# Kernel optimization log

Hardware: AMD Instinct MI355X
Metric: run time of the kernel (lower is better)

## Reference

```python
import jax, jax.numpy as jnp
import numpy as np

B, N, C_IN, C_OUT, R_IN, R_OUT, NUM_PSI, E = 4, 1024, 128, 256, 32, 32, 2, 65536


def psi(x, src, dst, W, b):
    # GIN-style GNN layer: aggregate neighbors via scatter-add, then linear+relu
    agg = jax.ops.segment_sum(x[src], dst, num_segments=x.shape[0])
    return jax.nn.relu((x + agg) @ W + b)


def setup_inputs() -> dict:
    key = jax.random.key(0)
    ks = jax.random.split(key, 12)
    inp = {
        'x_s': jax.random.normal(ks[0], (B * N, C_IN), jnp.float32),
        'edge_index_s': jax.random.randint(ks[1], (2, E), 0, B * N, jnp.int32),
        'x_t': jax.random.normal(ks[2], (B * N, C_IN), jnp.float32),
        'edge_index_t': jax.random.randint(ks[3], (2, E), 0, B * N, jnp.int32),
        'r': jax.random.normal(ks[4], (NUM_PSI, B, N, R_IN), jnp.float32),
        'W1': jax.random.normal(ks[5], (C_IN, C_OUT), jnp.float32) * (0.2 / np.sqrt(C_IN)),
        'b1': jnp.zeros((C_OUT,), jnp.float32),
        'Wp': jax.random.normal(ks[6], (NUM_PSI, R_IN, R_OUT), jnp.float32) * (1.0 / np.sqrt(R_IN)),
        'bp': jnp.zeros((NUM_PSI, R_OUT), jnp.float32),
        'Wm1': jax.random.normal(ks[7], (R_OUT, R_OUT), jnp.float32) * (1.0 / np.sqrt(R_OUT)),
        'bm1': jnp.zeros((R_OUT,), jnp.float32),
        'Wm2': jax.random.normal(ks[8], (R_OUT, 1), jnp.float32) * (1.0 / np.sqrt(R_OUT)),
        'bm2': jnp.zeros((1,), jnp.float32),
        'sum_weights': jnp.ones((NUM_PSI + 1,), jnp.float32),
    }
    return inp


def reference(x_s, edge_index_s, x_t, edge_index_t, r, W1, b1, Wp, bp, Wm1, bm1, Wm2, bm2, sum_weights):
    src_s, dst_s = edge_index_s[0], edge_index_s[1]
    src_t, dst_t = edge_index_t[0], edge_index_t[1]
    # psi_1 node embeddings, then dense-batch (equal-size graphs -> masks all true)
    h_s = psi(x_s, src_s, dst_s, W1, b1).reshape(B, N, C_OUT)
    h_t = psi(x_t, src_t, dst_t, W1, b1).reshape(B, N, C_OUT)
    S_hat = jnp.einsum('bsc,btc->bst', h_s, h_t)  # [B, N_s, N_t]
    S_0 = jax.nn.softmax(S_hat, axis=-1)
    S_stack = []
    for i in range(NUM_PSI):  # structurally distinct psi modules
        S = jax.nn.softmax(S_hat, axis=-1)
        r_s = r[i]  # [B, N, R_IN] random node indicators
        r_t = jnp.einsum('bst,bsr->btr', S, r_s)
        o_s = psi(r_s.reshape(B * N, R_IN), src_s, dst_s, Wp[i], bp[i]).reshape(B, N, R_OUT)
        o_t = psi(r_t.reshape(B * N, R_IN), src_t, dst_t, Wp[i], bp[i]).reshape(B, N, R_OUT)
        D = o_s[:, :, None, :] - o_t[:, None, :, :]  # [B, N_s, N_t, R_OUT]
        upd = (jax.nn.relu(D @ Wm1 + bm1) @ Wm2 + bm2)[..., 0]
        S_hat = S_hat + upd
        S_stack.append(jax.nn.softmax(S_hat, axis=-1))
    S_final = sum_weights[0] * S_0
    for i in range(NUM_PSI):
        S_final = S_final + sum_weights[i + 1] * S_stack[i]
    return jax.nn.softmax(S_final.reshape(B * N, N), axis=-1)
```

## Files before the change

kernel.cpp:

```cpp
#include <hip/hip_runtime.h>
#include <hip/hip_bf16.h>

#define NBATCH 4
#define NSEQ   1024
#define BNN    4096
#define CIN    128
#define COUT   256
#define RDIM   32
#define NEDGE  65536

__global__ void edge_hist(const int* __restrict__ ei_s, const int* __restrict__ ei_t,
                          int* __restrict__ cnt) {
    int gid = blockIdx.x * blockDim.x + threadIdx.x;
    int list = gid >> 16;
    int e = gid & (NEDGE - 1);
    const int* ei = list ? ei_t : ei_s;
    atomicAdd(&cnt[list * BNN + ei[NEDGE + e]], 1);
}

__global__ void edge_scan(const int* __restrict__ cnt, int* __restrict__ offs,
                          int* __restrict__ cursor) {
    __shared__ int sums[256];
    int list = blockIdx.x;
    int tid = threadIdx.x;
    int local[16];
    int s = 0;
#pragma unroll
    for (int k = 0; k < 16; k++) { local[k] = cnt[list * BNN + tid * 16 + k]; s += local[k]; }
    sums[tid] = s;
    __syncthreads();
    for (int off = 1; off < 256; off <<= 1) {
        int v = 0;
        if (tid >= off) v = sums[tid - off];
        __syncthreads();
        if (tid >= off) sums[tid] += v;
        __syncthreads();
    }
    int run = tid ? sums[tid - 1] : 0;
#pragma unroll
    for (int k = 0; k < 16; k++) {
        offs[list * (BNN + 1) + tid * 16 + k] = run;
        cursor[list * BNN + tid * 16 + k] = run;
        run += local[k];
    }
    if (tid == 255) offs[list * (BNN + 1) + BNN] = run;
}

__global__ void edge_place(const int* __restrict__ ei_s, const int* __restrict__ ei_t,
                           int* __restrict__ cursor, int* __restrict__ ssrc) {
    int gid = blockIdx.x * blockDim.x + threadIdx.x;
    int list = gid >> 16;
    int e = gid & (NEDGE - 1);
    const int* ei = list ? ei_t : ei_s;
    int dst = ei[NEDGE + e], src = ei[e];
    int p = atomicAdd(&cursor[list * BNN + dst], 1);
    ssrc[list * NEDGE + p] = src;
}

__global__ void gather_agg128(const float* __restrict__ x_s, const float* __restrict__ x_t,
                              const int* __restrict__ offs, const int* __restrict__ ssrc,
                              float* __restrict__ t_s, float* __restrict__ t_t) {
    __shared__ int sl[128];
    int node = blockIdx.x & (BNN - 1);
    int list = blockIdx.x >> 12;
    const float* x = list ? x_t : x_s;
    float* t = list ? t_t : t_s;
    int c = threadIdx.x;
    int beg = offs[list * (BNN + 1) + node], end = offs[list * (BNN + 1) + node + 1];
    float acc = x[(size_t)node * CIN + c];
    for (int base = beg; base < end; base += 128) {
        int cnt = min(128, end - base);
        __syncthreads();
        if (c < cnt) sl[c] = ssrc[list * NEDGE + base + c];
        __syncthreads();
        int e = 0;
        for (; e + 4 <= cnt; e += 4) {
            int n0 = sl[e], n1 = sl[e + 1], n2 = sl[e + 2], n3 = sl[e + 3];
            acc += x[(size_t)n0 * CIN + c] + x[(size_t)n1 * CIN + c]
                 + x[(size_t)n2 * CIN + c] + x[(size_t)n3 * CIN + c];
        }
        for (; e < cnt; e++) acc += x[(size_t)sl[e] * CIN + c];
    }
    t[(size_t)node * CIN + c] = acc;
}

__global__ void gather_agg32(const float* __restrict__ rs, const float* __restrict__ rtin,
                             const int* __restrict__ offs, const int* __restrict__ ssrc,
                             float* __restrict__ trs, float* __restrict__ trt) {
    int list = blockIdx.y;
    int node = blockIdx.x * 8 + (threadIdx.x >> 5);
    int c = threadIdx.x & 31;
    const float* in = list ? rtin : rs;
    float* outp = list ? trt : trs;
    int beg = offs[list * (BNN + 1) + node], end = offs[list * (BNN + 1) + node + 1];
    float acc = in[(size_t)node * RDIM + c];
    for (int e = beg; e < end; e++)
        acc += in[(size_t)ssrc[list * NEDGE + e] * RDIM + c];
    outp[(size_t)node * RDIM + c] = acc;
}

__global__ void psi1_gemm(const float* __restrict__ t_s, const float* __restrict__ t_t,
                          const float* __restrict__ W1, const float* __restrict__ b1,
                          float* __restrict__ h_s, float* __restrict__ h_t) {
    __shared__ float rows[8][CIN];
    int half = blockIdx.x >> 9;
    const float* t = half ? t_t : t_s;
    float* h = half ? h_t : h_s;
    int r0 = (blockIdx.x & 511) * 8;
    int tid = threadIdx.x;
    {
        int rr = tid >> 5, c4 = (tid & 31) << 2;
        *(float4*)&rows[rr][c4] = *(const float4*)(t + (size_t)(r0 + rr) * CIN + c4);
    }
    __syncthreads();
    float acc[8];
    float bias = b1[tid];
#pragma unroll
    for (int r = 0; r < 8; r++) acc[r] = bias;
    for (int k = 0; k < CIN; k++) {
        float w = W1[k * COUT + tid];
#pragma unroll
        for (int r = 0; r < 8; r++) acc[r] = fmaf(rows[r][k], w, acc[r]);
    }
#pragma unroll
    for (int r = 0; r < 8; r++)
        h[(size_t)(r0 + r) * COUT + tid] = fmaxf(acc[r], 0.f);
}

__global__ __launch_bounds__(256) void shat_gemm(const float* __restrict__ hs,
                                                 const float* __restrict__ ht,
                                                 float* __restrict__ Sh) {
    __shared__ float As[16][68];
    __shared__ float Bs[16][68];
    int flat = blockIdx.x;
    int swz = (flat & 7) * 128 + (flat >> 3);
    int bx = swz & 15, by = (swz >> 4) & 15, bz = swz >> 8;
    int b  = bz;
    int s0 = by * 64, t0 = bx * 64;
    const float* A  = hs + (size_t)b * NSEQ * COUT;
    const float* Bm = ht + (size_t)b * NSEQ * COUT;
    int tid = threadIdx.x;
    int tx = tid & 15, ty = tid >> 4;
    int lr = tid >> 2, lk = (tid & 3) << 2;
    const float* Ap = A  + (size_t)(s0 + lr) * COUT + lk;
    const float* Bp = Bm + (size_t)(t0 + lr) * COUT + lk;
    float4 a0 = *(const float4*)(Ap);
    float4 b0 = *(const float4*)(Bp);
    float acc[4][4] = {};
    for (int kp = 0; kp < 16; kp++) {
        __syncthreads();
        As[lk + 0][lr] = a0.x; As[lk + 1][lr] = a0.y;
        As[lk + 2][lr] = a0.z; As[lk + 3][lr] = a0.w;
        Bs[lk + 0][lr] = b0.x; Bs[lk + 1][lr] = b0.y;
        Bs[lk + 2][lr] = b0.z; Bs[lk + 3][lr] = b0.w;
        __syncthreads();
        if (kp < 15) {
            a0 = *(const float4*)(Ap + (kp + 1) * 16);
            b0 = *(const float4*)(Bp + (kp + 1) * 16);
        }
#pragma unroll
        for (int k = 0; k < 16; k++) {
            float av[4], bv[4];
            *(float4*)&av[0] = *(const float4*)&As[k][ty * 4];
            *(float4*)&bv[0] = *(const float4*)&Bs[k][tx * 4];
#pragma unroll
            for (int i = 0; i < 4; i++)
#pragma unroll
                for (int j = 0; j < 4; j++)
                    acc[i][j] = fmaf(av[i], bv[j], acc[i][j]);
        }
    }
#pragma unroll
    for (int i = 0; i < 4; i++) {
        float4 v = make_float4(acc[i][0], acc[i][1], acc[i][2], acc[i][3]);
        *(float4*)(Sh + ((size_t)b * NSEQ + s0 + ty * 4 + i) * NSEQ + t0 + tx * 4) = v;
    }
}

__global__ void softmax_stats(const float* __restrict__ Sh, float* __restrict__ mstat,
                              float* __restrict__ istat) {
    int row = blockIdx.x, tid = threadIdx.x;
    float4 v = *(const float4*)(Sh + (size_t)row * NSEQ + tid * 4);
    float m = fmaxf(fmaxf(v.x, v.y), fmaxf(v.z, v.w));
#pragma unroll
    for (int o = 32; o; o >>= 1) m = fmaxf(m, __shfl_xor(m, o));
    __shared__ float redm[4], reds[4];
    int wid = tid >> 6, lane = tid & 63;
    if (lane == 0) redm[wid] = m;
    __syncthreads();
    m = fmaxf(fmaxf(redm[0], redm[1]), fmaxf(redm[2], redm[3]));
    float s = __expf(v.x - m) + __expf(v.y - m) + __expf(v.z - m) + __expf(v.w - m);
#pragma unroll
    for (int o = 32; o; o >>= 1) s += __shfl_xor(s, o);
    if (lane == 0) reds[wid] = s;
    __syncthreads();
    if (tid == 0) {
        float tot = reds[0] + reds[1] + reds[2] + reds[3];
        mstat[row] = m;
        istat[row] = 1.0f / tot;
    }
}

__global__ void softmax_final3(const float* __restrict__ Sh0, const float* __restrict__ Sh1,
                               const float* __restrict__ Sh2, const float* __restrict__ m0a,
                               const float* __restrict__ i0a, const float* __restrict__ m1a,
                               const float* __restrict__ i1a, const float* __restrict__ sw,
                               float* __restrict__ out) {
    int row = blockIdx.x, tid = threadIdx.x;
    __shared__ float red[4];
    int wid = tid >> 6, lane = tid & 63;
    float4 v0 = *(const float4*)(Sh0 + (size_t)row * NSEQ + tid * 4);
    float4 v1 = *(const float4*)(Sh1 + (size_t)row * NSEQ + tid * 4);
    float4 v2 = *(const float4*)(Sh2 + (size_t)row * NSEQ + tid * 4);
    float m2 = fmaxf(fmaxf(v2.x, v2.y), fmaxf(v2.z, v2.w));
#pragma unroll
    for (int o = 32; o; o >>= 1) m2 = fmaxf(m2, __shfl_xor(m2, o));
    if (lane == 0) red[wid] = m2;
    __syncthreads();
    m2 = fmaxf(fmaxf(red[0], red[1]), fmaxf(red[2], red[3]));
    __syncthreads();
    float4 e2;
    e2.x = __expf(v2.x - m2); e2.y = __expf(v2.y - m2);
    e2.z = __expf(v2.z - m2); e2.w = __expf(v2.w - m2);
    float s2 = e2.x + e2.y + e2.z + e2.w;
#pragma unroll
    for (int o = 32; o; o >>= 1) s2 += __shfl_xor(s2, o);
    if (lane == 0) red[wid] = s2;
    __syncthreads();
    s2 = red[0] + red[1] + red[2] + red[3];
    __syncthreads();
    float w0 = sw[0] * i0a[row], w1 = sw[1] * i1a[row], w2 = sw[2] / s2;
    float m0 = m0a[row], m1 = m1a[row];
    float4 f;
    f.x = fmaf(w0, __expf(v0.x - m0), fmaf(w1, __expf(v1.x - m1), w2 * e2.x));
    f.y = fmaf(w0, __expf(v0.y - m0), fmaf(w1, __expf(v1.y - m1), w2 * e2.y));
    f.z = fmaf(w0, __expf(v0.z - m0), fmaf(w1, __expf(v1.z - m1), w2 * e2.z));
    f.w = fmaf(w0, __expf(v0.w - m0), fmaf(w1, __expf(v1.w - m1), w2 * e2.w));
    float mf = fmaxf(fmaxf(f.x, f.y), fmaxf(f.z, f.w));
#pragma unroll
    for (int o = 32; o; o >>= 1) mf = fmaxf(mf, __shfl_xor(mf, o));
    if (lane == 0) red[wid] = mf;
    __syncthreads();
    mf = fmaxf(fmaxf(red[0], red[1]), fmaxf(red[2], red[3]));
    __syncthreads();
    float4 ef;
    ef.x = __expf(f.x - mf); ef.y = __expf(f.y - mf);
    ef.z = __expf(f.z - mf); ef.w = __expf(f.w - mf);
    float sf = ef.x + ef.y + ef.z + ef.w;
#pragma unroll
    for (int o = 32; o; o >>= 1) sf += __shfl_xor(sf, o);
    if (lane == 0) red[wid] = sf;
    __syncthreads();
    sf = red[0] + red[1] + red[2] + red[3];
    float inv = 1.0f / sf;
    float4 sv = make_float4(ef.x * inv, ef.y * inv, ef.z * inv, ef.w * inv);
    *(float4*)(out + (size_t)row * NSEQ + tid * 4) = sv;
}

__global__ void rt_part(const float* __restrict__ Sh, const float* __restrict__ mstat,
                        const float* __restrict__ istat, const float* __restrict__ rs,
                        float* __restrict__ part) {
    __shared__ float rsld[64][33];
    __shared__ float ml[64], il[64];
    int b = blockIdx.z, t0 = blockIdx.y * 128, s0 = blockIdx.x * 64;
    int tid = threadIdx.x;
    if (tid < 64) ml[tid] = mstat[b * NSEQ + s0 + tid];
    else if (tid < 128) il[tid - 64] = istat[b * NSEQ + s0 + tid - 64];
#pragma unroll
    for (int q = 0; q < 2; q++) {
        int lid = (tid << 1) + q;
        int srow = lid >> 3, c4 = (lid & 7) << 2;
        float4 v = *(const float4*)(rs + ((size_t)b * NSEQ + s0 + srow) * RDIM + c4);
        rsld[srow][c4] = v.x; rsld[srow][c4 + 1] = v.y;
        rsld[srow][c4 + 2] = v.z; rsld[srow][c4 + 3] = v.w;
    }
    __syncthreads();
    int t = t0 + (tid & 127);
    int j0 = (tid >> 7) << 4;
    float acc[16] = {};
    const float* Sp = Sh + ((size_t)b * NSEQ + s0) * NSEQ + t;
#pragma unroll 8
    for (int s = 0; s < 64; s++) {
        float p = __expf(Sp[(size_t)s * NSEQ] - ml[s]) * il[s];
#pragma unroll
        for (int j = 0; j < 16; j++) acc[j] = fmaf(p, rsld[s][j0 + j], acc[j]);
    }
    float* pp = part + (((size_t)blockIdx.x * NBATCH + b) * NSEQ + t) * RDIM + j0;
#pragma unroll
    for (int j4 = 0; j4 < 16; j4 += 4)
        *(float4*)(pp + j4) = make_float4(acc[j4], acc[j4 + 1], acc[j4 + 2], acc[j4 + 3]);
}

__global__ void rt_reduce(const float* __restrict__ part, float* __restrict__ rt) {
    int i = blockIdx.x * blockDim.x + threadIdx.x;
    const float4* p = (const float4*)part + i;
    float4 a = make_float4(0.f, 0.f, 0.f, 0.f);
#pragma unroll
    for (int c = 0; c < 16; c++) {
        float4 v = p[(size_t)c * (BNN * RDIM / 4)];
        a.x += v.x; a.y += v.y; a.z += v.z; a.w += v.w;
    }
    ((float4*)rt)[i] = a;
}

__global__ void psi_r(const float* __restrict__ trs, const float* __restrict__ trt,
                      const float* __restrict__ Wp, const float* __restrict__ bp,
                      const float* __restrict__ Wm1, const float* __restrict__ bm1,
                      const float* __restrict__ Wm2,
                      float* __restrict__ Ps, float* __restrict__ Pt,
                      float* __restrict__ Aps, float* __restrict__ Apt) {
    __shared__ float sWp[32 * 32], sWm1[32 * 32];
    __shared__ float srow[8][33], so[8][33];
    __shared__ float swm2[32];
    int which = blockIdx.y;
    const float* t_r = which ? trt : trs;
    float* P = which ? Pt : Ps;
    float* A = which ? Apt : Aps;
    int tid = threadIdx.x;
#pragma unroll
    for (int q = 0; q < 4; q++) {
        sWp[tid + q * 256]  = Wp[tid + q * 256];
        sWm1[tid + q * 256] = Wm1[tid + q * 256];
    }
    if (tid < 32) swm2[tid] = Wm2[tid];
    int g = tid >> 5, j = tid & 31;
    int row = blockIdx.x * 8 + g;
    srow[g][j] = t_r[(size_t)row * RDIM + j];
    __syncthreads();
    float acc = bp[j];
#pragma unroll
    for (int k = 0; k < 32; k++) acc = fmaf(srow[g][k], sWp[k * 32 + j], acc);
    float o = fmaxf(acc, 0.f);
    so[g][j] = o;
    __syncthreads();
    float acc2 = which ? 0.f : bm1[j];
#pragma unroll
    for (int k = 0; k < 32; k++) acc2 = fmaf(so[g][k], sWm1[k * 32 + j], acc2);
    P[(size_t)row * RDIM + j] = acc2;
    float v = acc2 * swm2[j];
#pragma unroll
    for (int o2 = 16; o2; o2 >>= 1) v += __shfl_xor(v, o2, 32);
    if (j == 0) A[row] = v;
}

__global__ __launch_bounds__(256) void upd_add(const float* __restrict__ Ps,
                                               const float* __restrict__ Pt,
                                               const float* __restrict__ Aps,
                                               const float* __restrict__ Apt,
                                               const float* __restrict__ Wm2,
                                               const float* __restrict__ bm2p,
                                               const float* __restrict__ Shin,
                                               float* __restrict__ Shout) {
    __shared__ float sPsT[32][68];
    __shared__ float sPtT[32][68];
    __shared__ float swm[32];
    __shared__ float sAs[64], sAt[64];
    int b = blockIdx.z, s0 = blockIdx.y * 64, t0 = blockIdx.x * 64;
    int tid = threadIdx.x;
    {
        int lr = tid >> 2, lk = (tid & 3) << 3;
        const float* p = Ps + ((size_t)b * NSEQ + s0 + lr) * RDIM + lk;
        float4 v0 = *(const float4*)p, v1 = *(const float4*)(p + 4);
        sPsT[lk + 0][lr] = v0.x; sPsT[lk + 1][lr] = v0.y;
        sPsT[lk + 2][lr] = v0.z; sPsT[lk + 3][lr] = v0.w;
        sPsT[lk + 4][lr] = v1.x; sPsT[lk + 5][lr] = v1.y;
        sPsT[lk + 6][lr] = v1.z; sPsT[lk + 7][lr] = v1.w;
        const float* q = Pt + ((size_t)b * NSEQ + t0 + lr) * RDIM + lk;
        float4 u0 = *(const float4*)q, u1 = *(const float4*)(q + 4);
        sPtT[lk + 0][lr] = u0.x; sPtT[lk + 1][lr] = u0.y;
        sPtT[lk + 2][lr] = u0.z; sPtT[lk + 3][lr] = u0.w;
        sPtT[lk + 4][lr] = u1.x; sPtT[lk + 5][lr] = u1.y;
        sPtT[lk + 6][lr] = u1.z; sPtT[lk + 7][lr] = u1.w;
    }
    if (tid < 32) swm[tid] = Wm2[tid];
    else if (tid < 96)  sAs[tid - 32] = Aps[b * NSEQ + s0 + tid - 32];
    else if (tid < 160) sAt[tid - 96] = Apt[b * NSEQ + t0 + tid - 96];
    __syncthreads();
    int tx = tid & 15, ty = tid >> 4;
    float acc[4][4] = {};
#pragma unroll 8
    for (int k = 0; k < 32; k++) {
        float w = swm[k];
        float ps[4], pt[4];
        *(float4*)&ps[0] = *(const float4*)&sPsT[k][ty * 4];
        *(float4*)&pt[0] = *(const float4*)&sPtT[k][tx * 4];
#pragma unroll
        for (int i = 0; i < 4; i++)
#pragma unroll
            for (int j = 0; j < 4; j++)
                acc[i][j] = fmaf(fabsf(ps[i] - pt[j]), w, acc[i][j]);
    }
    float bm2 = bm2p[0];
#pragma unroll
    for (int i = 0; i < 4; i++) {
        float as = sAs[ty * 4 + i];
        size_t base = ((size_t)b * NSEQ + s0 + ty * 4 + i) * NSEQ + t0 + tx * 4;
        float4 old = *(const float4*)(Shin + base);
        float4 f;
        f.x = old.x + 0.5f * (acc[i][0] + as - sAt[tx * 4 + 0]) + bm2;
        f.y = old.y + 0.5f * (acc[i][1] + as - sAt[tx * 4 + 1]) + bm2;
        f.z = old.z + 0.5f * (acc[i][2] + as - sAt[tx * 4 + 2]) + bm2;
        f.w = old.w + 0.5f * (acc[i][3] + as - sAt[tx * 4 + 3]) + bm2;
        *(float4*)(Shout + base) = f;
    }
}

extern "C" void kernel_launch(void* const* d_in, const int* in_sizes, int n_in,
                              void* d_out, int out_size, void* d_ws, size_t ws_size,
                              hipStream_t stream) {
    const float* x_s  = (const float*)d_in[0];
    const int*   ei_s = (const int*)  d_in[1];
    const float* x_t  = (const float*)d_in[2];
    const int*   ei_t = (const int*)  d_in[3];
    const float* r    = (const float*)d_in[4];
    const float* W1   = (const float*)d_in[5];
    const float* b1   = (const float*)d_in[6];
    const float* Wp   = (const float*)d_in[7];
    const float* bp   = (const float*)d_in[8];
    const float* Wm1  = (const float*)d_in[9];
    const float* bm1  = (const float*)d_in[10];
    const float* Wm2  = (const float*)d_in[11];
    const float* bm2  = (const float*)d_in[12];
    const float* sw   = (const float*)d_in[13];
    float* out = (float*)d_out;

    float* ws = (float*)d_ws;
    float* t_s  = ws;  ws += (size_t)BNN * CIN;
    float* t_t  = ws;  ws += (size_t)BNN * CIN;
    float* h_s  = ws;  ws += (size_t)BNN * COUT;
    float* h_t  = ws;  ws += (size_t)BNN * COUT;
    float* Sh0  = ws;  ws += (size_t)NBATCH * NSEQ * NSEQ;
    float* Sh1  = ws;  ws += (size_t)NBATCH * NSEQ * NSEQ;
    float* Sh2  = ws;  ws += (size_t)NBATCH * NSEQ * NSEQ;
    float* mstat = ws; ws += 2 * BNN;
    float* istat = ws; ws += 2 * BNN;
    float* rt   = ws;  ws += (size_t)BNN * RDIM;
    float* trs  = ws;  ws += (size_t)BNN * RDIM;
    float* trt  = ws;  ws += (size_t)BNN * RDIM;
    float* Ps   = ws;  ws += (size_t)BNN * RDIM;
    float* Pt   = ws;  ws += (size_t)BNN * RDIM;
    float* Aps  = ws;  ws += BNN;
    float* Apt  = ws;  ws += BNN;
    int* icnt  = (int*)ws;
    int* ioffs = icnt  + 2 * BNN;
    int* icur  = ioffs + 2 * (BNN + 1);
    int* issrc = icur  + 2 * BNN;
    float* rtpart = h_s;

    float* ShA[3] = {Sh0, Sh1, Sh2};

    hipMemsetAsync(icnt, 0, 2 * BNN * sizeof(int), stream);
    edge_hist <<<512, 256, 0, stream>>>(ei_s, ei_t, icnt);
    edge_scan <<<2, 256, 0, stream>>>(icnt, ioffs, icur);
    edge_place<<<512, 256, 0, stream>>>(ei_s, ei_t, icur, issrc);

    gather_agg128<<<8192, 128, 0, stream>>>(x_s, x_t, ioffs, issrc, t_s, t_t);
    psi1_gemm<<<1024, 256, 0, stream>>>(t_s, t_t, W1, b1, h_s, h_t);
    shat_gemm<<<1024, 256, 0, stream>>>(h_s, h_t, Sh0);

    for (int i = 0; i < 2; i++) {
        softmax_stats<<<4096, 256, 0, stream>>>(ShA[i], mstat + i * BNN, istat + i * BNN);
        rt_part<<<dim3(16, 8, 4), 256, 0, stream>>>(ShA[i], mstat + i * BNN, istat + i * BNN,
                                                    r + (size_t)i * BNN * RDIM, rtpart);
        rt_reduce<<<128, 256, 0, stream>>>(rtpart, rt);
        gather_agg32<<<dim3(512, 2), 256, 0, stream>>>(r + (size_t)i * BNN * RDIM, rt,
                                                       ioffs, issrc, trs, trt);
        psi_r<<<dim3(512, 2), 256, 0, stream>>>(trs, trt, Wp + i * RDIM * RDIM,
                                                bp + i * RDIM, Wm1, bm1, Wm2,
                                                Ps, Pt, Aps, Apt);
        upd_add<<<dim3(16, 16, 4), 256, 0, stream>>>(Ps, Pt, Aps, Apt, Wm2, bm2,
                                                     ShA[i], ShA[i + 1]);
    }
    softmax_final3<<<4096, 256, 0, stream>>>(Sh0, Sh1, Sh2, mstat, istat,
                                             mstat + BNN, istat + BNN, sw, out);
}
```

Baseline: 203.7 us.

## Fuse softmax row statistics into GEMM and update epilogues via partial tile stats

Computes per-tile row max and sum-of-exponentials in the epilogues of shat_gemm and upd_add, then merges the 16 tile partials per row in a small stats_combine kernel. This removes the separate softmax_stats passes over the 16MB S_hat matrices, and softmax_final3 no longer has to compute Sh2's own max and sum. In exchange the epilogues do extra exp and shuffle work and write partial buffers, plus two extra tiny launches.

```diff
diff --git a/kernel.cpp b/kernel.cpp
--- a/kernel.cpp
+++ b/kernel.cpp
@@ -8,6 +8,7 @@
 #define COUT   256
 #define RDIM   32
 #define NEDGE  65536
+#define NTILE  16
 
 __global__ void edge_hist(const int* __restrict__ ei_s, const int* __restrict__ ei_t,
                           int* __restrict__ cnt) {
@@ -129,7 +130,9 @@
 
 __global__ __launch_bounds__(256) void shat_gemm(const float* __restrict__ hs,
                                                  const float* __restrict__ ht,
-                                                 float* __restrict__ Sh) {
+                                                 float* __restrict__ Sh,
+                                                 float* __restrict__ pmax,
+                                                 float* __restrict__ psum) {
     __shared__ float As[16][68];
     __shared__ float Bs[16][68];
     int flat = blockIdx.x;
@@ -174,84 +177,67 @@
     for (int i = 0; i < 4; i++) {
         float4 v = make_float4(acc[i][0], acc[i][1], acc[i][2], acc[i][3]);
         *(float4*)(Sh + ((size_t)b * NSEQ + s0 + ty * 4 + i) * NSEQ + t0 + tx * 4) = v;
-    }
-}
-
-__global__ void softmax_stats(const float* __restrict__ Sh, float* __restrict__ mstat,
-                              float* __restrict__ istat) {
-    int row = blockIdx.x, tid = threadIdx.x;
-    float4 v = *(const float4*)(Sh + (size_t)row * NSEQ + tid * 4);
-    float m = fmaxf(fmaxf(v.x, v.y), fmaxf(v.z, v.w));
-#pragma unroll
-    for (int o = 32; o; o >>= 1) m = fmaxf(m, __shfl_xor(m, o));
-    __shared__ float redm[4], reds[4];
-    int wid = tid >> 6, lane = tid & 63;
-    if (lane == 0) redm[wid] = m;
-    __syncthreads();
-    m = fmaxf(fmaxf(redm[0], redm[1]), fmaxf(redm[2], redm[3]));
-    float s = __expf(v.x - m) + __expf(v.y - m) + __expf(v.z - m) + __expf(v.w - m);
-#pragma unroll
-    for (int o = 32; o; o >>= 1) s += __shfl_xor(s, o);
-    if (lane == 0) reds[wid] = s;
-    __syncthreads();
-    if (tid == 0) {
-        float tot = reds[0] + reds[1] + reds[2] + reds[3];
-        mstat[row] = m;
-        istat[row] = 1.0f / tot;
-    }
+        float ml = fmaxf(fmaxf(v.x, v.y), fmaxf(v.z, v.w));
+#pragma unroll
+        for (int o = 1; o < 16; o <<= 1) ml = fmaxf(ml, __shfl_xor(ml, o, 16));
+        float sl = __expf(v.x - ml) + __expf(v.y - ml) + __expf(v.z - ml) + __expf(v.w - ml);
+#pragma unroll
+        for (int o = 1; o < 16; o <<= 1) sl += __shfl_xor(sl, o, 16);
+        if (tx == 0) {
+            int grow = b * NSEQ + s0 + ty * 4 + i;
+            pmax[grow * NTILE + bx] = ml;
+            psum[grow * NTILE + bx] = sl;
+        }
+    }
+}
+
+__global__ void stats_combine(const float* __restrict__ pmax, const float* __restrict__ psum,
+                              float* __restrict__ mstat, float* __restrict__ istat) {
+    int row = blockIdx.x * blockDim.x + threadIdx.x;
+    float pm[NTILE];
+    float m = -3.4e38f;
+#pragma unroll
+    for (int t = 0; t < NTILE; t++) { pm[t] = pmax[row * NTILE + t]; m = fmaxf(m, pm[t]); }
+    float s = 0.f;
+#pragma unroll
+    for (int t = 0; t < NTILE; t++) s += psum[row * NTILE + t] * __expf(pm[t] - m);
+    mstat[row] = m;
+    istat[row] = 1.0f / s;
 }
 
 __global__ void softmax_final3(const float* __restrict__ Sh0, const float* __restrict__ Sh1,
-                               const float* __restrict__ Sh2, const float* __restrict__ m0a,
-                               const float* __restrict__ i0a, const float* __restrict__ m1a,
-                               const float* __restrict__ i1a, const float* __restrict__ sw,
+                               const float* __restrict__ Sh2, const float* __restrict__ mst,
+                               const float* __restrict__ ist, const float* __restrict__ sw,
                                float* __restrict__ out) {
     int row = blockIdx.x, tid = threadIdx.x;
-    __shared__ float red[4];
+    __shared__ float redm[4], reds[4];
     int wid = tid >> 6, lane = tid & 63;
     float4 v0 = *(const float4*)(Sh0 + (size_t)row * NSEQ + tid * 4);
     float4 v1 = *(const float4*)(Sh1 + (size_t)row * NSEQ + tid * 4);
     float4 v2 = *(const float4*)(Sh2 + (size_t)row * NSEQ + tid * 4);
-    float m2 = fmaxf(fmaxf(v2.x, v2.y), fmaxf(v2.z, v2.w));
-#pragma unroll
-    for (int o = 32; o; o >>= 1) m2 = fmaxf(m2, __shfl_xor(m2, o));
-    if (lane == 0) red[wid] = m2;
-    __syncthreads();
-    m2 = fmaxf(fmaxf(red[0], red[1]), fmaxf(red[2], red[3]));
-    __syncthreads();
-    float4 e2;
-    e2.x = __expf(v2.x - m2); e2.y = __expf(v2.y - m2);
-    e2.z = __expf(v2.z - m2); e2.w = __expf(v2.w - m2);
-    float s2 = e2.x + e2.y + e2.z + e2.w;
-#pragma unroll
-    for (int o = 32; o; o >>= 1) s2 += __shfl_xor(s2, o);
-    if (lane == 0) red[wid] = s2;
-    __syncthreads();
-    s2 = red[0] + red[1] + red[2] + red[3];
-    __syncthreads();
-    float w0 = sw[0] * i0a[row], w1 = sw[1] * i1a[row], w2 = sw[2] / s2;
-    float m0 = m0a[row], m1 = m1a[row];
+    float m0 = mst[row],           w0 = sw[0] * ist[row];
+    float m1 = mst[BNN + row],     w1 = sw[1] * ist[BNN + row];
+    float m2 = mst[2 * BNN + row], w2 = sw[2] * ist[2 * BNN + row];
     float4 f;
-    f.x = fmaf(w0, __expf(v0.x - m0), fmaf(w1, __expf(v1.x - m1), w2 * e2.x));
-    f.y = fmaf(w0, __expf(v0.y - m0), fmaf(w1, __expf(v1.y - m1), w2 * e2.y));
-    f.z = fmaf(w0, __expf(v0.z - m0), fmaf(w1, __expf(v1.z - m1), w2 * e2.z));
-    f.w = fmaf(w0, __expf(v0.w - m0), fmaf(w1, __expf(v1.w - m1), w2 * e2.w));
+    f.x = fmaf(w0, __expf(v0.x - m0), fmaf(w1, __expf(v1.x - m1), w2 * __expf(v2.x - m2)));
+    f.y = fmaf(w0, __expf(v0.y - m0), fmaf(w1, __expf(v1.y - m1), w2 * __expf(v2.y - m2)));
+    f.z = fmaf(w0, __expf(v0.z - m0), fmaf(w1, __expf(v1.z - m1), w2 * __expf(v2.z - m2)));
+    f.w = fmaf(w0, __expf(v0.w - m0), fmaf(w1, __expf(v1.w - m1), w2 * __expf(v2.w - m2)));
     float mf = fmaxf(fmaxf(f.x, f.y), fmaxf(f.z, f.w));
 #pragma unroll
     for (int o = 32; o; o >>= 1) mf = fmaxf(mf, __shfl_xor(mf, o));
-    if (lane == 0) red[wid] = mf;
-    __syncthreads();
-    mf = fmaxf(fmaxf(red[0], red[1]), fmaxf(red[2], red[3]));
-    __syncthreads();
+    if (lane == 0) redm[wid] = mf;
+    __syncthreads();
+    mf = fmaxf(fmaxf(redm[0], redm[1]), fmaxf(redm[2], redm[3]));
     float4 ef;
     ef.x = __expf(f.x - mf); ef.y = __expf(f.y - mf);
     ef.z = __expf(f.z - mf); ef.w = __expf(f.w - mf);
     float sf = ef.x + ef.y + ef.z + ef.w;
 #pragma unroll
     for (int o = 32; o; o >>= 1) sf += __shfl_xor(sf, o);
-    if (lane == 0) red[wid] = sf;
-    __syncthreads();
-    sf = red[0] + red[1] + red[2] + red[3];
+    if (lane == 0) reds[wid] = sf;
+    __syncthreads();
+    sf = reds[0] + reds[1] + reds[2] + reds[3];
     float inv = 1.0f / sf;
     float4 sv = make_float4(ef.x * inv, ef.y * inv, ef.z * inv, ef.w * inv);
     *(float4*)(out + (size_t)row * NSEQ + tid * 4) = sv;
@@ -343,14 +329,16 @@
     if (j == 0) A[row] = v;
 }
 
-__global__ __launch_bounds__(256) void upd_add(const float* __restrict__ Ps,
-                                               const float* __restrict__ Pt,
-                                               const float* __restrict__ Aps,
-                                               const float* __restrict__ Apt,
-                                               const float* __restrict__ Wm2,
-                                               const float* __restrict__ bm2p,
-                                               const float* __restrict__ Shin,
-                                               float* __restrict__ Shout) {
+__global__ __launch_bounds__(256) void upd_add_stats(const float* __restrict__ Ps,
+                                                     const float* __restrict__ Pt,
+                                                     const float* __restrict__ Aps,
+                                                     const float* __restrict__ Apt,
+                                                     const float* __restrict__ Wm2,
+                                                     const float* __restrict__ bm2p,
+                                                     const float* __restrict__ Shin,
+                                                     float* __restrict__ Shout,
+                                                     float* __restrict__ pmax,
+                                                     float* __restrict__ psum) {
     __shared__ float sPsT[32][68];
     __shared__ float sPtT[32][68];
     __shared__ float swm[32];
@@ -402,6 +390,17 @@
         f.z = old.z + 0.5f * (acc[i][2] + as - sAt[tx * 4 + 2]) + bm2;
         f.w = old.w + 0.5f * (acc[i][3] + as - sAt[tx * 4 + 3]) + bm2;
         *(float4*)(Shout + base) = f;
+        float ml = fmaxf(fmaxf(f.x, f.y), fmaxf(f.z, f.w));
+#pragma unroll
+        for (int o = 1; o < 16; o <<= 1) ml = fmaxf(ml, __shfl_xor(ml, o, 16));
+        float sl = __expf(f.x - ml) + __expf(f.y - ml) + __expf(f.z - ml) + __expf(f.w - ml);
+#pragma unroll
+        for (int o = 1; o < 16; o <<= 1) sl += __shfl_xor(sl, o, 16);
+        if (tx == 0) {
+            int grow = b * NSEQ + s0 + ty * 4 + i;
+            pmax[grow * NTILE + blockIdx.x] = ml;
+            psum[grow * NTILE + blockIdx.x] = sl;
+        }
     }
 }
 
@@ -432,8 +431,10 @@
     float* Sh0  = ws;  ws += (size_t)NBATCH * NSEQ * NSEQ;
     float* Sh1  = ws;  ws += (size_t)NBATCH * NSEQ * NSEQ;
     float* Sh2  = ws;  ws += (size_t)NBATCH * NSEQ * NSEQ;
-    float* mstat = ws; ws += 2 * BNN;
-    float* istat = ws; ws += 2 * BNN;
+    float* mstat = ws; ws += 3 * BNN;
+    float* istat = ws; ws += 3 * BNN;
+    float* pmax = ws;  ws += (size_t)BNN * NTILE;
+    float* psum = ws;  ws += (size_t)BNN * NTILE;
     float* rt   = ws;  ws += (size_t)BNN * RDIM;
     float* trs  = ws;  ws += (size_t)BNN * RDIM;
     float* trt  = ws;  ws += (size_t)BNN * RDIM;
@@ -456,10 +457,10 @@
 
     gather_agg128<<<8192, 128, 0, stream>>>(x_s, x_t, ioffs, issrc, t_s, t_t);
     psi1_gemm<<<1024, 256, 0, stream>>>(t_s, t_t, W1, b1, h_s, h_t);
-    shat_gemm<<<1024, 256, 0, stream>>>(h_s, h_t, Sh0);
+    shat_gemm<<<1024, 256, 0, stream>>>(h_s, h_t, Sh0, pmax, psum);
+    stats_combine<<<16, 256, 0, stream>>>(pmax, psum, mstat, istat);
 
     for (int i = 0; i < 2; i++) {
-        softmax_stats<<<4096, 256, 0, stream>>>(ShA[i], mstat + i * BNN, istat + i * BNN);
         rt_part<<<dim3(16, 8, 4), 256, 0, stream>>>(ShA[i], mstat + i * BNN, istat + i * BNN,
                                                     r + (size_t)i * BNN * RDIM, rtpart);
         rt_reduce<<<128, 256, 0, stream>>>(rtpart, rt);
@@ -468,9 +469,10 @@
         psi_r<<<dim3(512, 2), 256, 0, stream>>>(trs, trt, Wp + i * RDIM * RDIM,
                                                 bp + i * RDIM, Wm1, bm1, Wm2,
                                                 Ps, Pt, Aps, Apt);
-        upd_add<<<dim3(16, 16, 4), 256, 0, stream>>>(Ps, Pt, Aps, Apt, Wm2, bm2,
-                                                     ShA[i], ShA[i + 1]);
-    }
-    softmax_final3<<<4096, 256, 0, stream>>>(Sh0, Sh1, Sh2, mstat, istat,
-                                             mstat + BNN, istat + BNN, sw, out);
-}
+        upd_add_stats<<<dim3(16, 16, 4), 256, 0, stream>>>(Ps, Pt, Aps, Apt, Wm2, bm2,
+                                                           ShA[i], ShA[i + 1], pmax, psum);
+        stats_combine<<<16, 256, 0, stream>>>(pmax, psum, mstat + (i + 1) * BNN,
+                                              istat + (i + 1) * BNN);
+    }
+    softmax_final3<<<4096, 256, 0, stream>>>(Sh0, Sh1, Sh2, mstat, istat, sw, out);
+}
```

Result: no change. 206.7 us (+1.5%).

## Compute S_hat GEMM with split-bf16 MFMA instead of fp32 FMA

Applied to the files above, without the earlier changes.

The psi1 GEMM now writes its output as high and low bf16 halves. The S_hat batched GEMM uses the 16x16x32 bf16 MFMA instruction with three products (hi*hi, hi*lo, lo*hi) to approximate fp32 accuracy. This replaces the shared-memory tiled fp32 FMA kernel, aiming to move the largest GEMM onto the matrix cores. In exchange it loses the LDS reuse, so each wave loads its operands straight from global memory, and precision drops slightly. The rtpart scratch buffer now gets its own workspace region, since the h buffers are no longer reused for it.

```diff
diff --git a/kernel.cpp b/kernel.cpp
--- a/kernel.cpp
+++ b/kernel.cpp
@@ -8,6 +8,9 @@
 #define COUT   256
 #define RDIM   32
 #define NEDGE  65536
+
+typedef __attribute__((ext_vector_type(8))) short bf16x8;
+typedef __attribute__((ext_vector_type(4))) float f32x4;
 
 __global__ void edge_hist(const int* __restrict__ ei_s, const int* __restrict__ ei_t,
                           int* __restrict__ cnt) {
@@ -101,11 +104,13 @@
 
 __global__ void psi1_gemm(const float* __restrict__ t_s, const float* __restrict__ t_t,
                           const float* __restrict__ W1, const float* __restrict__ b1,
-                          float* __restrict__ h_s, float* __restrict__ h_t) {
+                          unsigned short* __restrict__ hhi_s, unsigned short* __restrict__ hlo_s,
+                          unsigned short* __restrict__ hhi_t, unsigned short* __restrict__ hlo_t) {
     __shared__ float rows[8][CIN];
     int half = blockIdx.x >> 9;
     const float* t = half ? t_t : t_s;
-    float* h = half ? h_t : h_s;
+    unsigned short* hhi = half ? hhi_t : hhi_s;
+    unsigned short* hlo = half ? hlo_t : hlo_s;
     int r0 = (blockIdx.x & 511) * 8;
     int tid = threadIdx.x;
     {
@@ -123,58 +128,55 @@
         for (int r = 0; r < 8; r++) acc[r] = fmaf(rows[r][k], w, acc[r]);
     }
 #pragma unroll
-    for (int r = 0; r < 8; r++)
-        h[(size_t)(r0 + r) * COUT + tid] = fmaxf(acc[r], 0.f);
-}
-
-__global__ __launch_bounds__(256) void shat_gemm(const float* __restrict__ hs,
-                                                 const float* __restrict__ ht,
+    for (int r = 0; r < 8; r++) {
+        float o = fmaxf(acc[r], 0.f);
+        __hip_bfloat16 bh = __float2bfloat16(o);
+        float rhi = __bfloat162float(bh);
+        __hip_bfloat16 bl = __float2bfloat16(o - rhi);
+        size_t idx = (size_t)(r0 + r) * COUT + tid;
+        hhi[idx] = *(unsigned short*)&bh;
+        hlo[idx] = *(unsigned short*)&bl;
+    }
+}
+
+__global__ __launch_bounds__(256) void shat_mfma(const unsigned short* __restrict__ hhi_s,
+                                                 const unsigned short* __restrict__ hlo_s,
+                                                 const unsigned short* __restrict__ hhi_t,
+                                                 const unsigned short* __restrict__ hlo_t,
                                                  float* __restrict__ Sh) {
-    __shared__ float As[16][68];
-    __shared__ float Bs[16][68];
     int flat = blockIdx.x;
     int swz = (flat & 7) * 128 + (flat >> 3);
-    int bx = swz & 15, by = (swz >> 4) & 15, bz = swz >> 8;
-    int b  = bz;
+    int bx = swz & 15, by = (swz >> 4) & 15, b = swz >> 8;
     int s0 = by * 64, t0 = bx * 64;
-    const float* A  = hs + (size_t)b * NSEQ * COUT;
-    const float* Bm = ht + (size_t)b * NSEQ * COUT;
-    int tid = threadIdx.x;
-    int tx = tid & 15, ty = tid >> 4;
-    int lr = tid >> 2, lk = (tid & 3) << 2;
-    const float* Ap = A  + (size_t)(s0 + lr) * COUT + lk;
-    const float* Bp = Bm + (size_t)(t0 + lr) * COUT + lk;
-    float4 a0 = *(const float4*)(Ap);
-    float4 b0 = *(const float4*)(Bp);
-    float acc[4][4] = {};
-    for (int kp = 0; kp < 16; kp++) {
-        __syncthreads();
-        As[lk + 0][lr] = a0.x; As[lk + 1][lr] = a0.y;
-        As[lk + 2][lr] = a0.z; As[lk + 3][lr] = a0.w;
-        Bs[lk + 0][lr] = b0.x; Bs[lk + 1][lr] = b0.y;
-        Bs[lk + 2][lr] = b0.z; Bs[lk + 3][lr] = b0.w;
-        __syncthreads();
-        if (kp < 15) {
-            a0 = *(const float4*)(Ap + (kp + 1) * 16);
-            b0 = *(const float4*)(Bp + (kp + 1) * 16);
+    int tid = threadIdx.x;
+    int wave = tid >> 6, lane = tid & 63;
+    int l15 = lane & 15;
+    int koff = (lane >> 4) * 8;
+    size_t arow = ((size_t)b * NSEQ + s0 + wave * 16 + l15) * COUT + koff;
+    const unsigned short* pAhi = hhi_s + arow;
+    const unsigned short* pAlo = hlo_s + arow;
+    size_t brow = ((size_t)b * NSEQ + t0 + l15) * COUT + koff;
+    const unsigned short* pBhi = hhi_t + brow;
+    const unsigned short* pBlo = hlo_t + brow;
+    f32x4 acc[4] = {};
+    for (int k0 = 0; k0 < COUT; k0 += 32) {
+        bf16x8 ahi = *(const bf16x8*)(pAhi + k0);
+        bf16x8 alo = *(const bf16x8*)(pAlo + k0);
+#pragma unroll
+        for (int j = 0; j < 4; j++) {
+            bf16x8 bhi = *(const bf16x8*)(pBhi + (size_t)j * 16 * COUT + k0);
+            bf16x8 blo = *(const bf16x8*)(pBlo + (size_t)j * 16 * COUT + k0);
+            acc[j] = __builtin_amdgcn_mfma_f32_16x16x32_bf16(ahi, bhi, acc[j], 0, 0, 0);
+            acc[j] = __builtin_amdgcn_mfma_f32_16x16x32_bf16(ahi, blo, acc[j], 0, 0, 0);
+            acc[j] = __builtin_amdgcn_mfma_f32_16x16x32_bf16(alo, bhi, acc[j], 0, 0, 0);
         }
-#pragma unroll
-        for (int k = 0; k < 16; k++) {
-            float av[4], bv[4];
-            *(float4*)&av[0] = *(const float4*)&As[k][ty * 4];
-            *(float4*)&bv[0] = *(const float4*)&Bs[k][tx * 4];
-#pragma unroll
-            for (int i = 0; i < 4; i++)
-#pragma unroll
-                for (int j = 0; j < 4; j++)
-                    acc[i][j] = fmaf(av[i], bv[j], acc[i][j]);
-        }
-    }
-#pragma unroll
-    for (int i = 0; i < 4; i++) {
-        float4 v = make_float4(acc[i][0], acc[i][1], acc[i][2], acc[i][3]);
-        *(float4*)(Sh + ((size_t)b * NSEQ + s0 + ty * 4 + i) * NSEQ + t0 + tx * 4) = v;
-    }
+    }
+    int rbase = s0 + wave * 16 + (lane >> 4) * 4;
+#pragma unroll
+    for (int j = 0; j < 4; j++)
+#pragma unroll
+        for (int r = 0; r < 4; r++)
+            Sh[((size_t)b * NSEQ + rbase + r) * NSEQ + t0 + j * 16 + l15] = acc[j][r];
 }
 
 __global__ void softmax_stats(const float* __restrict__ Sh, float* __restrict__ mstat,
@@ -427,8 +429,12 @@
     float* ws = (float*)d_ws;
     float* t_s  = ws;  ws += (size_t)BNN * CIN;
     float* t_t  = ws;  ws += (size_t)BNN * CIN;
-    float* h_s  = ws;  ws += (size_t)BNN * COUT;
-    float* h_t  = ws;  ws += (size_t)BNN * COUT;
+    unsigned short* hhi_s = (unsigned short*)ws;
+    unsigned short* hlo_s = hhi_s + (size_t)BNN * COUT;
+    unsigned short* hhi_t = hlo_s + (size_t)BNN * COUT;
+    unsigned short* hlo_t = hhi_t + (size_t)BNN * COUT;
+    ws += (size_t)BNN * COUT * 2;
+    float* rtpart = ws; ws += (size_t)16 * BNN * RDIM;
     float* Sh0  = ws;  ws += (size_t)NBATCH * NSEQ * NSEQ;
     float* Sh1  = ws;  ws += (size_t)NBATCH * NSEQ * NSEQ;
     float* Sh2  = ws;  ws += (size_t)NBATCH * NSEQ * NSEQ;
@@ -445,7 +451,6 @@
     int* ioffs = icnt  + 2 * BNN;
     int* icur  = ioffs + 2 * (BNN + 1);
     int* issrc = icur  + 2 * BNN;
-    float* rtpart = h_s;
 
     float* ShA[3] = {Sh0, Sh1, Sh2};
 
@@ -455,8 +460,8 @@
     edge_place<<<512, 256, 0, stream>>>(ei_s, ei_t, icur, issrc);
 
     gather_agg128<<<8192, 128, 0, stream>>>(x_s, x_t, ioffs, issrc, t_s, t_t);
-    psi1_gemm<<<1024, 256, 0, stream>>>(t_s, t_t, W1, b1, h_s, h_t);
-    shat_gemm<<<1024, 256, 0, stream>>>(h_s, h_t, Sh0);
+    psi1_gemm<<<1024, 256, 0, stream>>>(t_s, t_t, W1, b1, hhi_s, hlo_s, hhi_t, hlo_t);
+    shat_mfma<<<1024, 256, 0, stream>>>(hhi_s, hlo_s, hhi_t, hlo_t, Sh0);
 
     for (int i = 0; i < 2; i++) {
         softmax_stats<<<4096, 256, 0, stream>>>(ShA[i], mstat + i * BNN, istat + i * BNN);
```

After: 211.9 us. 4.0% more time.
